# Performance work log

Hardware: AMD Instinct MI355X
Metric: run time of the kernel (lower is better)

Reference implementation:

```python
import jax, jax.numpy as jnp
import numpy as np

K = 3          # kernel_size
STRIDE = 1
ITERS = 3      # num_iterations


def _squash(t, axis=-1):
    sn = jnp.sum(t * t, axis=axis, keepdims=True)
    return sn / (1.0 + sn) * t / jnp.sqrt(sn)


def setup_inputs() -> dict:
    key = jax.random.key(0)
    k1, k2 = jax.random.split(key)
    x = jax.random.normal(k1, (4, 32, 14, 14, 8), dtype=jnp.float32)
    # route_weights: [num_capsules, num_in_capsules*K*K, in_channels, out_channels]
    route_weights = jax.random.normal(k2, (32, 32 * K * K, 8, 16), dtype=jnp.float32)
    bias = jnp.zeros((32, 16), dtype=jnp.float32)  # torch init fills with 0.0
    return {"x": x, "route_weights": route_weights, "bias": bias}


def reference(x, route_weights, bias):
    B, Ci, H, W_, Cin = x.shape
    A, N, _, D = route_weights.shape  # num_capsules, route_nodes, in_ch, out_ch
    w = (H - K) // STRIDE + 1
    # Extract all KxK windows at once. idx: [w, K]
    idx = jnp.arange(w)[:, None] * STRIDE + jnp.arange(K)[None, :]
    # xw: [B, Ci, w, K, w, K, Cin]
    xw = x[:, :, idx[:, :, None, None], idx[None, None, :, :], :]
    # -> [B, w, w, Ci*K*K, Cin]; node ordering (Ci, K, K) matches torch .view
    xw = xw.transpose(0, 2, 4, 1, 3, 5, 6).reshape(B, w, w, Ci * K * K, Cin)
    # priors: [A, B, w, w, N, D]
    priors = jnp.einsum('bijnc,ancd->abijnd', xw, route_weights)
    # logits broadcast over D in the original (delta has trailing dim 1),
    # so keep them as scalars per route node: [A, B, w, w, N]
    logits = jnp.zeros((A, B, w, w, N), dtype=priors.dtype)
    b = bias[:, None, None, None, :]  # [A,1,1,1,D]
    out = None
    for i in range(ITERS):
        probs = jax.nn.softmax(logits, axis=-1)  # softmax over route nodes (dim=2 in torch)
        s = jnp.einsum('abijn,abijnd->abijd', probs, priors) + b
        out = _squash(s)
        if i != ITERS - 1:
            logits = logits + jnp.einsum('abijnd,abijd->abijn', priors, out)
    # torch permutes (num_caps, B, w, w, D) -> (B, num_caps, w, w, D)
    return out.transpose(1, 0, 2, 3, 4)
```

## Files before the change

kernel.cpp:

```cpp
#include <hip/hip_runtime.h>

#define W_OUT 12
#define N_CAPS 288
#define CIN 8
#define DD 16
#define A_DIM 32
#define B_DIM 4
#define CI 32
#define H_IN 14
#define NT 18
#define XSTRIDE 12
#define NROWS 576
#define WCHUNK 2048

__device__ __forceinline__ float4 shfl_xor4(float4 v, int m) {
    float4 r;
    r.x = __shfl_xor(v.x, m);
    r.y = __shfl_xor(v.y, m);
    r.z = __shfl_xor(v.z, m);
    r.w = __shfl_xor(v.w, m);
    return r;
}

__device__ __forceinline__ void stage_piece(const float* g, float* lds) {
    __builtin_amdgcn_global_load_lds(
        (const __attribute__((address_space(1))) void*)g,
        (__attribute__((address_space(3))) void*)lds, 16, 0, 0);
}

__global__ __launch_bounds__(256, 3) void capsule_kernel(
    const float* __restrict__ x,
    const float* __restrict__ Wt,
    const float* __restrict__ bias,
    float* __restrict__ out)
{
    __shared__ __align__(16) float xs[NROWS * XSTRIDE];
    __shared__ __align__(16) float wbuf[2][WCHUNK];
    __shared__ int xoff[N_CAPS];

    const int tid = threadIdx.x;
    int bid = blockIdx.x;
    const int jb = bid % 3; bid /= 3;
    const int i  = bid % W_OUT; bid /= W_OUT;
    const int b  = bid % B_DIM; bid /= B_DIM;
    const int a  = bid;
    const int j0 = jb * 4;

    const int lane = tid & 63;
    const int wv   = tid >> 6;
    const int dq   = lane & 3;
    const int nr   = lane >> 2;
    const int swz  = nr & 7;

    const float* Wa = Wt + (size_t)a * (N_CAPS * CIN * DD);

    auto issue_stage = [&](int t, int buf) {
        #pragma unroll
        for (int k = 0; k < 2; ++k) {
            int p  = wv * 2 + k;
            int L  = p * 64 + lane;
            int nl = L >> 5;
            int G  = (L & ~31) | ((L & 31) ^ (nl & 7));
            stage_piece(Wa + (size_t)t * WCHUNK + (size_t)G * 4, &wbuf[buf][p * 256]);
        }
    };

    for (int n = tid; n < N_CAPS; n += 256) {
        int ci = n / 9, r = n % 9;
        xoff[n] = (ci * 18 + (r / 3) * 6 + (r % 3)) * XSTRIDE;
    }

    issue_stage(0, 0);

    for (int row = tid; row < NROWS; row += 256) {
        int ci = row / 18, rr = row % 18;
        int ki = rr / 6, jj = rr % 6;
        const float* src = x + ((((size_t)b * CI + ci) * H_IN + (i + ki)) * H_IN + (j0 + jj)) * CIN;
        float4 v0 = *reinterpret_cast<const float4*>(src);
        float4 v1 = *reinterpret_cast<const float4*>(src + 4);
        float* dst = &xs[row * XSTRIDE];
        *reinterpret_cast<float4*>(dst)     = v0;
        *reinterpret_cast<float4*>(dst + 4) = v1;
    }
    const float4 bv = *reinterpret_cast<const float4*>(bias + a * DD + dq * 4);
    __syncthreads();
    issue_stage(1, 1);

    const int sjoff = wv * XSTRIDE;

    float4 ps[NT];
    #pragma unroll
    for (int t = 0; t < NT; ++t) {
        if (t < NT - 1) { asm volatile("s_waitcnt vmcnt(2)" ::: "memory"); }
        else            { asm volatile("s_waitcnt vmcnt(0)" ::: "memory"); }
        __builtin_amdgcn_sched_barrier(0);
        __builtin_amdgcn_s_barrier();
        __builtin_amdgcn_sched_barrier(0);

        const int n = nr + 16 * t;
        const float* xp = &xs[xoff[n] + sjoff];
        float xr[CIN];
        *reinterpret_cast<float4*>(&xr[0]) = *reinterpret_cast<const float4*>(xp);
        *reinterpret_cast<float4*>(&xr[4]) = *reinterpret_cast<const float4*>(xp + 4);

        const float4* wb = reinterpret_cast<const float4*>(&wbuf[t & 1][0]);
        float4 acc = {0.f, 0.f, 0.f, 0.f};
        #pragma unroll
        for (int c = 0; c < CIN; ++c) {
            float4 w4 = wb[nr * 32 + (((c << 2) | dq) ^ swz)];
            acc.x = fmaf(xr[c], w4.x, acc.x);
            acc.y = fmaf(xr[c], w4.y, acc.y);
            acc.z = fmaf(xr[c], w4.z, acc.z);
            acc.w = fmaf(xr[c], w4.w, acc.w);
        }
        ps[t] = acc;

        __builtin_amdgcn_sched_barrier(0);
        __builtin_amdgcn_s_barrier();
        __builtin_amdgcn_sched_barrier(0);
        if (t + 2 < NT) issue_stage(t + 2, t & 1);
    }

    float lt[NT];
    float4 out4;

    {
        float4 s = {0.f, 0.f, 0.f, 0.f};
        #pragma unroll
        for (int t = 0; t < NT; ++t) {
            s.x += ps[t].x; s.y += ps[t].y; s.z += ps[t].z; s.w += ps[t].w;
        }
        #pragma unroll
        for (int m = 4; m <= 32; m <<= 1) { float4 o = shfl_xor4(s, m); s.x += o.x; s.y += o.y; s.z += o.z; s.w += o.w; }
        const float inv0 = 1.0f / 288.0f;
        s.x = fmaf(s.x, inv0, bv.x); s.y = fmaf(s.y, inv0, bv.y);
        s.z = fmaf(s.z, inv0, bv.z); s.w = fmaf(s.w, inv0, bv.w);
        float sn = s.x*s.x + s.y*s.y + s.z*s.z + s.w*s.w;
        sn += __shfl_xor(sn, 1); sn += __shfl_xor(sn, 2);
        float factor = sn / (1.0f + sn) * rsqrtf(sn);
        out4.x = factor * s.x; out4.y = factor * s.y; out4.z = factor * s.z; out4.w = factor * s.w;

        #pragma unroll
        for (int t = 0; t < NT; ++t) {
            float p = ps[t].x*out4.x + ps[t].y*out4.y + ps[t].z*out4.z + ps[t].w*out4.w;
            p += __shfl_xor(p, 1);
            p += __shfl_xor(p, 2);
            lt[t] = p;
        }
    }

    #pragma unroll
    for (int it = 1; it < 3; ++it) {
        float m = -1e30f;
        #pragma unroll
        for (int t = 0; t < NT; ++t) m = fmaxf(m, lt[t]);
        #pragma unroll
        for (int msk = 4; msk <= 32; msk <<= 1) m = fmaxf(m, __shfl_xor(m, msk));
        float e[NT];
        float se = 0.f;
        #pragma unroll
        for (int t = 0; t < NT; ++t) { e[t] = __expf(lt[t] - m); se += e[t]; }
        #pragma unroll
        for (int msk = 4; msk <= 32; msk <<= 1) se += __shfl_xor(se, msk);
        const float inv = 1.0f / se;

        float4 s = {0.f, 0.f, 0.f, 0.f};
        #pragma unroll
        for (int t = 0; t < NT; ++t) {
            s.x = fmaf(e[t], ps[t].x, s.x); s.y = fmaf(e[t], ps[t].y, s.y);
            s.z = fmaf(e[t], ps[t].z, s.z); s.w = fmaf(e[t], ps[t].w, s.w);
        }
        #pragma unroll
        for (int msk = 4; msk <= 32; msk <<= 1) { float4 o = shfl_xor4(s, msk); s.x += o.x; s.y += o.y; s.z += o.z; s.w += o.w; }
        s.x = fmaf(s.x, inv, bv.x); s.y = fmaf(s.y, inv, bv.y);
        s.z = fmaf(s.z, inv, bv.z); s.w = fmaf(s.w, inv, bv.w);

        float sn = s.x*s.x + s.y*s.y + s.z*s.z + s.w*s.w;
        sn += __shfl_xor(sn, 1); sn += __shfl_xor(sn, 2);
        float factor = sn / (1.0f + sn) * rsqrtf(sn);
        out4.x = factor * s.x; out4.y = factor * s.y; out4.z = factor * s.z; out4.w = factor * s.w;

        if (it != 2) {
            #pragma unroll
            for (int t = 0; t < NT; ++t) {
                float p = ps[t].x*out4.x + ps[t].y*out4.y + ps[t].z*out4.z + ps[t].w*out4.w;
                p += __shfl_xor(p, 1);
                p += __shfl_xor(p, 2);
                lt[t] += p;
            }
        }
    }

    if (nr == 0) {
        size_t o = ((((size_t)b * A_DIM + a) * W_OUT + i) * W_OUT + (j0 + wv)) * DD + dq * 4;
        *reinterpret_cast<float4*>(out + o) = out4;
    }
}

extern "C" void kernel_launch(void* const* d_in, const int* in_sizes, int n_in,
                              void* d_out, int out_size, void* d_ws, size_t ws_size,
                              hipStream_t stream) {
    const float* x    = (const float*)d_in[0];
    const float* Wt   = (const float*)d_in[1];
    const float* bias = (const float*)d_in[2];
    float* out = (float*)d_out;
    (void)in_sizes; (void)n_in; (void)out_size; (void)d_ws; (void)ws_size;

    const int grid = A_DIM * B_DIM * W_OUT * 3;
    capsule_kernel<<<grid, 256, 0, stream>>>(x, Wt, bias, out);
}
```

Measured before the change: 155.4 us.

## Stage weight tiles three at a time with c-major LDS layout

The weight pipeline is restructured so each double-buffered stage loads three route-node tiles instead of one. This cuts the number of block-wide barriers and waitcnt points in the prior-computation loop from two per tile to two per stage. The LDS weight layout changes to c-major, so each lane reads one contiguous float4 and the XOR swizzle is no longer needed. The larger LDS footprint costs occupancy, so launch bounds drop from 3 to 2 blocks per CU, which leaves less room to hide latency across blocks.

```diff
diff --git a/kernel.cpp b/kernel.cpp
--- a/kernel.cpp
+++ b/kernel.cpp
@@ -11,7 +11,9 @@
 #define NT 18
 #define XSTRIDE 12
 #define NROWS 576
-#define WCHUNK 2048
+#define TS_F 2048
+#define CH 3
+#define NSTG 6
 
 __device__ __forceinline__ float4 shfl_xor4(float4 v, int m) {
     float4 r;
@@ -28,14 +30,14 @@
         (__attribute__((address_space(3))) void*)lds, 16, 0, 0);
 }
 
-__global__ __launch_bounds__(256, 3) void capsule_kernel(
+__global__ __launch_bounds__(256, 2) void capsule_kernel(
     const float* __restrict__ x,
     const float* __restrict__ Wt,
     const float* __restrict__ bias,
     float* __restrict__ out)
 {
     __shared__ __align__(16) float xs[NROWS * XSTRIDE];
-    __shared__ __align__(16) float wbuf[2][WCHUNK];
+    __shared__ __align__(16) float wbuf[2][CH * TS_F];
     __shared__ int xoff[N_CAPS];
 
     const int tid = threadIdx.x;
@@ -50,28 +52,28 @@
     const int wv   = tid >> 6;
     const int dq   = lane & 3;
     const int nr   = lane >> 2;
-    const int swz  = nr & 7;
 
     const float* Wa = Wt + (size_t)a * (N_CAPS * CIN * DD);
 
-    auto issue_stage = [&](int t, int buf) {
-        #pragma unroll
-        for (int k = 0; k < 2; ++k) {
-            int p  = wv * 2 + k;
-            int L  = p * 64 + lane;
-            int nl = L >> 5;
-            int G  = (L & ~31) | ((L & 31) ^ (nl & 7));
-            stage_piece(Wa + (size_t)t * WCHUNK + (size_t)G * 4, &wbuf[buf][p * 256]);
+    const int g0 = (lane >> 2) * 128 + (lane & 3) * 4;
+    auto issue_chunk = [&](int t0, int buf) {
+        #pragma unroll
+        for (int k = 0; k < CH; ++k) {
+            const float* base = Wa + (size_t)(t0 + k) * TS_F;
+            #pragma unroll
+            for (int q = 0; q < 2; ++q) {
+                const int p = wv * 2 + q;
+                stage_piece(base + g0 + p * 16, &wbuf[buf][k * TS_F + p * 256]);
+            }
         }
     };
+
+    issue_chunk(0, 0);
 
     for (int n = tid; n < N_CAPS; n += 256) {
         int ci = n / 9, r = n % 9;
         xoff[n] = (ci * 18 + (r / 3) * 6 + (r % 3)) * XSTRIDE;
     }
-
-    issue_stage(0, 0);
-
     for (int row = tid; row < NROWS; row += 256) {
         int ci = row / 18, rr = row % 18;
         int ki = rr / 6, jj = rr % 6;
@@ -84,41 +86,45 @@
     }
     const float4 bv = *reinterpret_cast<const float4*>(bias + a * DD + dq * 4);
     __syncthreads();
-    issue_stage(1, 1);
+    issue_chunk(CH, 1);
 
     const int sjoff = wv * XSTRIDE;
 
     float4 ps[NT];
     #pragma unroll
-    for (int t = 0; t < NT; ++t) {
-        if (t < NT - 1) { asm volatile("s_waitcnt vmcnt(2)" ::: "memory"); }
-        else            { asm volatile("s_waitcnt vmcnt(0)" ::: "memory"); }
-        __builtin_amdgcn_sched_barrier(0);
-        __builtin_amdgcn_s_barrier();
-        __builtin_amdgcn_sched_barrier(0);
-
-        const int n = nr + 16 * t;
-        const float* xp = &xs[xoff[n] + sjoff];
-        float xr[CIN];
-        *reinterpret_cast<float4*>(&xr[0]) = *reinterpret_cast<const float4*>(xp);
-        *reinterpret_cast<float4*>(&xr[4]) = *reinterpret_cast<const float4*>(xp + 4);
-
-        const float4* wb = reinterpret_cast<const float4*>(&wbuf[t & 1][0]);
-        float4 acc = {0.f, 0.f, 0.f, 0.f};
-        #pragma unroll
-        for (int c = 0; c < CIN; ++c) {
-            float4 w4 = wb[nr * 32 + (((c << 2) | dq) ^ swz)];
-            acc.x = fmaf(xr[c], w4.x, acc.x);
-            acc.y = fmaf(xr[c], w4.y, acc.y);
-            acc.z = fmaf(xr[c], w4.z, acc.z);
-            acc.w = fmaf(xr[c], w4.w, acc.w);
-        }
-        ps[t] = acc;
-
-        __builtin_amdgcn_sched_barrier(0);
-        __builtin_amdgcn_s_barrier();
-        __builtin_amdgcn_sched_barrier(0);
-        if (t + 2 < NT) issue_stage(t + 2, t & 1);
+    for (int s = 0; s < NSTG; ++s) {
+        #pragma unroll
+        for (int k = 0; k < CH; ++k) {
+            const int t = s * CH + k;
+            const int n = nr + 16 * t;
+            const float* xp = &xs[xoff[n] + sjoff];
+            float xr[CIN];
+            *reinterpret_cast<float4*>(&xr[0]) = *reinterpret_cast<const float4*>(xp);
+            *reinterpret_cast<float4*>(&xr[4]) = *reinterpret_cast<const float4*>(xp + 4);
+            const float4* wb4 = reinterpret_cast<const float4*>(&wbuf[s & 1][k * TS_F]);
+            float4 acc = {0.f, 0.f, 0.f, 0.f};
+            #pragma unroll
+            for (int c = 0; c < CIN; ++c) {
+                float4 w4 = wb4[c * 64 + lane];
+                acc.x = fmaf(xr[c], w4.x, acc.x);
+                acc.y = fmaf(xr[c], w4.y, acc.y);
+                acc.z = fmaf(xr[c], w4.z, acc.z);
+                acc.w = fmaf(xr[c], w4.w, acc.w);
+            }
+            ps[t] = acc;
+        }
+        if (s < NSTG - 1) {
+            asm volatile("s_waitcnt lgkmcnt(0)" ::: "memory");
+            __builtin_amdgcn_s_barrier();
+            if (s + 2 < NSTG) {
+                issue_chunk((s + 2) * CH, s & 1);
+                asm volatile("s_waitcnt vmcnt(6)" ::: "memory");
+            } else {
+                asm volatile("s_waitcnt vmcnt(0)" ::: "memory");
+            }
+            __builtin_amdgcn_s_barrier();
+            __builtin_amdgcn_sched_barrier(0);
+        }
     }
 
     float lt[NT];
```

Result: no change. 153.6 us (-1.1%).
